# Kernel optimization log

Hardware: AMD Instinct MI355X
Metric: run time of the kernel (lower is better)

## Reference

```python
import jax, jax.numpy as jnp
import numpy as np

NB_KERNEL = 100
DIM_PER_KERNEL = 5


def setup_inputs() -> dict:
    key = jax.random.key(0)
    k1, k2 = jax.random.split(key)
    B, F = 1024, 1024
    x = jax.random.normal(k1, (B, F), dtype=jnp.float32)
    T = jax.random.normal(k2, (F, NB_KERNEL * DIM_PER_KERNEL), dtype=jnp.float32)
    return {"x": x, "T": T}


def reference(x, T):
    B = x.shape[0]
    # project: [B, F] @ [F, K*D] -> [B, K, D]
    m = (x @ T).reshape(B, NB_KERNEL, DIM_PER_KERNEL)
    # pairwise L1 distance over D between all batch rows: [B, K, B]
    # diffs[i, k, d, j] = m[i, k, d] - m[j, k, d]
    diffs = m[:, :, :, None] - jnp.transpose(m, (1, 2, 0))[None, :, :, :]
    l1 = jnp.sum(jnp.abs(diffs), axis=2)  # [B, K, B]
    # exp-kernel similarity summed across batch (includes self term exp(0)=1)
    feat = jnp.sum(jnp.exp(-l1), axis=2)  # [B, K]
    return jnp.concatenate([x, feat], axis=1)  # [B, F + K]
```

## Files before the change

kernel.cpp:

```cpp
#include <hip/hip_runtime.h>
#include <hip/hip_bf16.h>
#include <math.h>

#define B_SZ   1024
#define F_SZ   1024
#define NKER   100
#define DKER   5
#define CCOLS  (NKER * DKER)
#define OUTW   (F_SZ + NKER)
#define LOG2E_F 1.44269504088896340736f

typedef __attribute__((ext_vector_type(8))) short bf16x8;
typedef __attribute__((ext_vector_type(4))) float f32x4;

__device__ __forceinline__ float exp2_hw(float x) {
    float r;
    asm("v_exp_f32 %0, %1" : "=v"(r) : "v"(x));
    return r;
}
__device__ __forceinline__ unsigned cvt_pk_bf16(float lo, float hi) {
    unsigned r;
    asm("v_cvt_pk_bf16_f32 %0, %1, %2" : "=v"(r) : "v"(lo), "v"(hi));
    return r;
}

__global__ __launch_bounds__(256) void init_kernel(const float* __restrict__ x,
                                                   float* __restrict__ out) {
    const int row = blockIdx.x;
    const int t = threadIdx.x;
    const float4 v = *reinterpret_cast<const float4*>(&x[row * F_SZ + t * 4]);
    *reinterpret_cast<float4*>(&out[row * OUTW + t * 4]) = v;
}

__global__ __launch_bounds__(256) void stage_xb_kernel(const float* __restrict__ x,
                                                       short* __restrict__ xb) {
    const int tid = blockIdx.x * 256 + threadIdx.x;
    const int l = tid & 63;
    const int g = tid >> 6;
    const int jt = g >> 5, s = g & 31;
    const int j = jt * 16 + (l & 15);
    const int kb = s * 32 + (l >> 4) * 8;
    const float4 v0 = *reinterpret_cast<const float4*>(&x[j * F_SZ + kb]);
    const float4 v1 = *reinterpret_cast<const float4*>(&x[j * F_SZ + kb + 4]);
    uint4 w;
    w.x = cvt_pk_bf16(v0.x, v0.y);
    w.y = cvt_pk_bf16(v0.z, v0.w);
    w.z = cvt_pk_bf16(v1.x, v1.y);
    w.w = cvt_pk_bf16(v1.z, v1.w);
    *reinterpret_cast<uint4*>(&xb[(size_t)g * 512 + l * 8]) = w;
}

__global__ __launch_bounds__(256) void gemm_frag_kernel(const float* __restrict__ T,
                                                        const short* __restrict__ xb,
                                                        float* __restrict__ mt) {
    const int tid = threadIdx.x;
    const int l = tid & 63;
    const int w = tid >> 6;
    const int tile = blockIdx.x * 4 + w;
    const int ct = tile & 31, jt = tile >> 5;
    const int lr = l & 15;
    const int lk = (l >> 4) * 8;
    const int cA = ct * 16 + lr;
    const int cL = (cA < CCOLS) ? cA : (CCOLS - 1);

    const float* ap = T + (size_t)lk * CCOLS + cL;
    const short* bp = xb + ((size_t)(jt * 32) * 512 + l * 8);

    f32x4 acc = {0.f, 0.f, 0.f, 0.f};
    #pragma unroll 4
    for (int s = 0; s < 32; ++s) {
        const float a0 = ap[0 * CCOLS], a1 = ap[1 * CCOLS];
        const float a2 = ap[2 * CCOLS], a3 = ap[3 * CCOLS];
        const float a4 = ap[4 * CCOLS], a5 = ap[5 * CCOLS];
        const float a6 = ap[6 * CCOLS], a7 = ap[7 * CCOLS];
        const bf16x8 bf = *reinterpret_cast<const bf16x8*>(bp);
        ap += 32 * CCOLS;
        bp += 512;
        union { unsigned u[4]; bf16x8 v; } A;
        A.u[0] = cvt_pk_bf16(a0, a1);
        A.u[1] = cvt_pk_bf16(a2, a3);
        A.u[2] = cvt_pk_bf16(a4, a5);
        A.u[3] = cvt_pk_bf16(a6, a7);
        acc = __builtin_amdgcn_mfma_f32_16x16x32_bf16(A.v, bf, acc, 0, 0, 0);
    }

    const int jst = jt * 16 + lr;
    const int cst = ct * 16 + (l >> 4) * 4;
    #pragma unroll
    for (int q = 0; q < 4; ++q) {
        const int c = cst + q;
        if (c < CCOLS) mt[c * B_SZ + jst] = acc[q] * LOG2E_F;
    }
}

#define GAPAD 40

__global__ __launch_bounds__(512) void gemm_block_kernel(const float* __restrict__ x,
                                                         const float* __restrict__ T,
                                                         float* __restrict__ mt) {
    __shared__ short Al[2][32][GAPAD];
    __shared__ short Bl[2][32][GAPAD];
    __shared__ float red[4][64][4];
    const int tid = threadIdx.x;
    const int l = tid & 63;
    const int w = tid >> 6;
    const int h = tid >> 8;
    const int ht = tid & 255;
    const int c0 = blockIdx.x * 32;
    const int j0 = blockIdx.y * 32;
    const int fh = h * (F_SZ / 2);

    const int sac = ht & 31;
    const int sak = (ht >> 5) * 4;
    const int cldA = (c0 + sac < CCOLS) ? (c0 + sac) : (CCOLS - 1);
    const int sbj = ht >> 3;
    const int sbk = (ht & 7) * 4;

    const int q = w & 3;
    const int cq = (q & 1) * 16;
    const int jq = (q >> 1) * 16;
    const int fr = (l >> 4) * 8;
    const int ar = cq + (l & 15);
    const int br = jq + (l & 15);

    f32x4 acc = {0.f, 0.f, 0.f, 0.f};

    for (int s = 0; s < 16; ++s) {
        const int fb = fh + s * 32;
        const float a0 = T[(fb + sak + 0) * CCOLS + cldA];
        const float a1 = T[(fb + sak + 1) * CCOLS + cldA];
        const float a2 = T[(fb + sak + 2) * CCOLS + cldA];
        const float a3 = T[(fb + sak + 3) * CCOLS + cldA];
        const float4 b = *reinterpret_cast<const float4*>(&x[(j0 + sbj) * F_SZ + fb + sbk]);
        if (s) __syncthreads();
        {
            uint2 aw; aw.x = cvt_pk_bf16(a0, a1); aw.y = cvt_pk_bf16(a2, a3);
            *reinterpret_cast<uint2*>(&Al[h][sac][sak]) = aw;
            uint2 bw; bw.x = cvt_pk_bf16(b.x, b.y); bw.y = cvt_pk_bf16(b.z, b.w);
            *reinterpret_cast<uint2*>(&Bl[h][sbj][sbk]) = bw;
        }
        __syncthreads();
        const bf16x8 af = *reinterpret_cast<const bf16x8*>(&Al[h][ar][fr]);
        const bf16x8 bf = *reinterpret_cast<const bf16x8*>(&Bl[h][br][fr]);
        acc = __builtin_amdgcn_mfma_f32_16x16x32_bf16(af, bf, acc, 0, 0, 0);
    }

    if (h == 1) {
        #pragma unroll
        for (int qq = 0; qq < 4; ++qq) red[q][l][qq] = acc[qq];
    }
    __syncthreads();
    if (h == 0) {
        const int jst = j0 + jq + (l & 15);
        const int cst = c0 + cq + (l >> 4) * 4;
        #pragma unroll
        for (int qq = 0; qq < 4; ++qq) {
            const int c = cst + qq;
            if (c < CCOLS)
                mt[c * B_SZ + jst] = (acc[qq] + red[q][l][qq]) * LOG2E_F;
        }
    }
}

__global__ __launch_bounds__(256) void pair_kernel(const float* __restrict__ mt,
                                                   float* __restrict__ out) {
    __shared__ float red[256];
    const int tid = threadIdx.x;
    const int bx = blockIdx.x;
    const int k = blockIdx.y;
    const int cb = k * DKER;
    const int lane = tid & 63;
    const int wu = __builtin_amdgcn_readfirstlane(tid >> 6);
    const int i = bx * 64 + lane;

    const float a0 = mt[(cb + 0) * B_SZ + i];
    const float a1 = mt[(cb + 1) * B_SZ + i];
    const float a2 = mt[(cb + 2) * B_SZ + i];
    const float a3 = mt[(cb + 3) * B_SZ + i];
    const float a4 = mt[(cb + 4) * B_SZ + i];

    unsigned long long base =
        (unsigned long long)(uintptr_t)(mt + (size_t)cb * B_SZ + wu * 256);

    float acc = 0.f;
    for (int jb = 0; jb < 64; ++jb) {
        f32x4 q0, q1, q2, q3, q4;
        asm("s_load_dwordx4 %0, %[p], 0x0\n\t"
            "s_load_dwordx4 %1, %[p], 0x1000\n\t"
            "s_load_dwordx4 %2, %[p], 0x2000\n\t"
            "s_load_dwordx4 %3, %[p], 0x3000\n\t"
            "s_load_dwordx4 %4, %[p], 0x4000\n\t"
            "s_waitcnt lgkmcnt(0)"
            : "=s"(q0), "=s"(q1), "=s"(q2), "=s"(q3), "=s"(q4)
            : [p] "s"(base));
#define DOJ(E) { \
        const float d0 = q0[E] - a0; \
        const float d1 = q1[E] - a1; \
        const float d2 = q2[E] - a2; \
        const float d3 = q3[E] - a3; \
        const float d4 = q4[E] - a4; \
        const float p01 = fabsf(d0) + fabsf(d1); \
        const float p23 = fabsf(d2) + fabsf(d3); \
        const float p234 = p23 + fabsf(d4); \
        acc += exp2_hw(-p01 - p234); }
        DOJ(0) DOJ(1) DOJ(2) DOJ(3)
#undef DOJ
        base += 16;
    }

    red[tid] = acc;
    __syncthreads();
    if (tid < 64) {
        const float s = red[tid] + red[tid + 64] + red[tid + 128] + red[tid + 192];
        out[(bx * 64 + tid) * OUTW + F_SZ + k] = s;
    }
}

extern "C" void kernel_launch(void* const* d_in, const int* in_sizes, int n_in,
                              void* d_out, int out_size, void* d_ws, size_t ws_size,
                              hipStream_t stream) {
    const float* x = (const float*)d_in[0];
    const float* T = (const float*)d_in[1];
    float* out = (float*)d_out;
    float* mt = (float*)d_ws;
    short* xb = (short*)((char*)d_ws + (size_t)CCOLS * B_SZ * sizeof(float));

    const size_t need = (size_t)CCOLS * B_SZ * sizeof(float)
                      + (size_t)2048 * 512 * sizeof(short);

    init_kernel<<<dim3(B_SZ), 256, 0, stream>>>(x, out);
    if (ws_size >= need) {
        stage_xb_kernel<<<dim3(512), 256, 0, stream>>>(x, xb);
        gemm_frag_kernel<<<dim3(512), 256, 0, stream>>>(T, xb, mt);
    } else {
        gemm_block_kernel<<<dim3(16, 32), 512, 0, stream>>>(x, T, mt);
    }
    pair_kernel<<<dim3(B_SZ / 64, NKER), 256, 0, stream>>>(mt, out);
}
```

Baseline: 115.9 us.

## Pre-stage T into bf16 MFMA fragment layout and widen pair-kernel unrolling

Adds a kernel that transposes T through shared memory and converts it to bf16 MFMA fragments ahead of time, so the GEMM loads packed fragments instead of eight strided fp32 values per step. The pair kernel now loads two groups of scalar vectors per iteration and keeps two accumulators, halving the loop trip count and shortening the dependency chain. The negation is folded into the v_exp operand modifier. The cost is an extra launch and more workspace; if the workspace is too small, the fallback path is taken.

```diff
diff --git a/kernel.cpp b/kernel.cpp
--- a/kernel.cpp
+++ b/kernel.cpp
@@ -13,9 +13,9 @@
 typedef __attribute__((ext_vector_type(8))) short bf16x8;
 typedef __attribute__((ext_vector_type(4))) float f32x4;
 
-__device__ __forceinline__ float exp2_hw(float x) {
+__device__ __forceinline__ float exp2_neg_hw(float x) {
     float r;
-    asm("v_exp_f32 %0, %1" : "=v"(r) : "v"(x));
+    asm("v_exp_f32 %0, -%1" : "=v"(r) : "v"(x));
     return r;
 }
 __device__ __forceinline__ unsigned cvt_pk_bf16(float lo, float hi) {
@@ -50,41 +50,62 @@
     *reinterpret_cast<uint4*>(&xb[(size_t)g * 512 + l * 8]) = w;
 }
 
-__global__ __launch_bounds__(256) void gemm_frag_kernel(const float* __restrict__ T,
-                                                        const short* __restrict__ xb,
-                                                        float* __restrict__ mt) {
+__global__ __launch_bounds__(256) void stage_tb_kernel(const float* __restrict__ T,
+                                                       short* __restrict__ Tb) {
+    __shared__ float Tl[32][72];
+    const int t = threadIdx.x;
+    const int cg = blockIdx.x;
+    const int s = blockIdx.y;
+    const int k0 = s * 32;
+
+    const int kk = t >> 3;
+    const int cc8 = (t & 7) * 8;
+    #pragma unroll
+    for (int e = 0; e < 8; ++e) {
+        int c = cg * 64 + cc8 + e;
+        c = (c < CCOLS) ? c : (CCOLS - 1);
+        Tl[kk][cc8 + e] = T[(k0 + kk) * CCOLS + c];
+    }
+    __syncthreads();
+
+    const int l = t & 63;
+    const int ctl = t >> 6;
+    const int ctg = cg * 4 + ctl;
+    float v[8];
+    #pragma unroll
+    for (int e = 0; e < 8; ++e)
+        v[e] = Tl[(l >> 4) * 8 + e][ctl * 16 + (l & 15)];
+    uint4 w;
+    w.x = cvt_pk_bf16(v[0], v[1]);
+    w.y = cvt_pk_bf16(v[2], v[3]);
+    w.z = cvt_pk_bf16(v[4], v[5]);
+    w.w = cvt_pk_bf16(v[6], v[7]);
+    *reinterpret_cast<uint4*>(&Tb[((size_t)ctg * 32 + s) * 512 + l * 8]) = w;
+}
+
+__global__ __launch_bounds__(256) void gemm_frag2_kernel(const short* __restrict__ Tb,
+                                                         const short* __restrict__ xb,
+                                                         float* __restrict__ mt) {
     const int tid = threadIdx.x;
     const int l = tid & 63;
     const int w = tid >> 6;
     const int tile = blockIdx.x * 4 + w;
     const int ct = tile & 31, jt = tile >> 5;
-    const int lr = l & 15;
-    const int lk = (l >> 4) * 8;
-    const int cA = ct * 16 + lr;
-    const int cL = (cA < CCOLS) ? cA : (CCOLS - 1);
-
-    const float* ap = T + (size_t)lk * CCOLS + cL;
-    const short* bp = xb + ((size_t)(jt * 32) * 512 + l * 8);
+
+    const short* ap = Tb + ((size_t)ct * 32) * 512 + l * 8;
+    const short* bp = xb + ((size_t)jt * 32) * 512 + l * 8;
 
     f32x4 acc = {0.f, 0.f, 0.f, 0.f};
-    #pragma unroll 4
+    #pragma unroll 8
     for (int s = 0; s < 32; ++s) {
-        const float a0 = ap[0 * CCOLS], a1 = ap[1 * CCOLS];
-        const float a2 = ap[2 * CCOLS], a3 = ap[3 * CCOLS];
-        const float a4 = ap[4 * CCOLS], a5 = ap[5 * CCOLS];
-        const float a6 = ap[6 * CCOLS], a7 = ap[7 * CCOLS];
+        const bf16x8 af = *reinterpret_cast<const bf16x8*>(ap);
         const bf16x8 bf = *reinterpret_cast<const bf16x8*>(bp);
-        ap += 32 * CCOLS;
+        ap += 512;
         bp += 512;
-        union { unsigned u[4]; bf16x8 v; } A;
-        A.u[0] = cvt_pk_bf16(a0, a1);
-        A.u[1] = cvt_pk_bf16(a2, a3);
-        A.u[2] = cvt_pk_bf16(a4, a5);
-        A.u[3] = cvt_pk_bf16(a6, a7);
-        acc = __builtin_amdgcn_mfma_f32_16x16x32_bf16(A.v, bf, acc, 0, 0, 0);
-    }
-
-    const int jst = jt * 16 + lr;
+        acc = __builtin_amdgcn_mfma_f32_16x16x32_bf16(af, bf, acc, 0, 0, 0);
+    }
+
+    const int jst = jt * 16 + (l & 15);
     const int cst = ct * 16 + (l >> 4) * 4;
     #pragma unroll
     for (int q = 0; q < 4; ++q) {
@@ -182,33 +203,46 @@
     unsigned long long base =
         (unsigned long long)(uintptr_t)(mt + (size_t)cb * B_SZ + wu * 256);
 
-    float acc = 0.f;
-    for (int jb = 0; jb < 64; ++jb) {
-        f32x4 q0, q1, q2, q3, q4;
+    float accA = 0.f, accB = 0.f;
+    for (int jb = 0; jb < 32; ++jb) {
+        f32x4 q0, q1, q2, q3, q4, q5, q6, q7, q8, q9;
         asm("s_load_dwordx4 %0, %[p], 0x0\n\t"
             "s_load_dwordx4 %1, %[p], 0x1000\n\t"
             "s_load_dwordx4 %2, %[p], 0x2000\n\t"
             "s_load_dwordx4 %3, %[p], 0x3000\n\t"
             "s_load_dwordx4 %4, %[p], 0x4000\n\t"
+            "s_load_dwordx4 %5, %[p], 0x10\n\t"
+            "s_load_dwordx4 %6, %[p], 0x1010\n\t"
+            "s_load_dwordx4 %7, %[p], 0x2010\n\t"
+            "s_load_dwordx4 %8, %[p], 0x3010\n\t"
+            "s_load_dwordx4 %9, %[p], 0x4010\n\t"
             "s_waitcnt lgkmcnt(0)"
-            : "=s"(q0), "=s"(q1), "=s"(q2), "=s"(q3), "=s"(q4)
+            : "=&s"(q0), "=&s"(q1), "=&s"(q2), "=&s"(q3), "=&s"(q4),
+              "=&s"(q5), "=&s"(q6), "=&s"(q7), "=&s"(q8), "=&s"(q9)
             : [p] "s"(base));
-#define DOJ(E) { \
-        const float d0 = q0[E] - a0; \
-        const float d1 = q1[E] - a1; \
-        const float d2 = q2[E] - a2; \
-        const float d3 = q3[E] - a3; \
-        const float d4 = q4[E] - a4; \
+#define DOJ(Q0, Q1, Q2, Q3, Q4, E, ACC) { \
+        const float d0 = Q0[E] - a0; \
+        const float d1 = Q1[E] - a1; \
+        const float d2 = Q2[E] - a2; \
+        const float d3 = Q3[E] - a3; \
+        const float d4 = Q4[E] - a4; \
         const float p01 = fabsf(d0) + fabsf(d1); \
         const float p23 = fabsf(d2) + fabsf(d3); \
         const float p234 = p23 + fabsf(d4); \
-        acc += exp2_hw(-p01 - p234); }
-        DOJ(0) DOJ(1) DOJ(2) DOJ(3)
+        ACC += exp2_neg_hw(p01 + p234); }
+        DOJ(q0, q1, q2, q3, q4, 0, accA)
+        DOJ(q0, q1, q2, q3, q4, 1, accB)
+        DOJ(q0, q1, q2, q3, q4, 2, accA)
+        DOJ(q0, q1, q2, q3, q4, 3, accB)
+        DOJ(q5, q6, q7, q8, q9, 0, accA)
+        DOJ(q5, q6, q7, q8, q9, 1, accB)
+        DOJ(q5, q6, q7, q8, q9, 2, accA)
+        DOJ(q5, q6, q7, q8, q9, 3, accB)
 #undef DOJ
-        base += 16;
-    }
-
-    red[tid] = acc;
+        base += 32;
+    }
+
+    red[tid] = accA + accB;
     __syncthreads();
     if (tid < 64) {
         const float s = red[tid] + red[tid + 64] + red[tid + 128] + red[tid + 192];
@@ -222,16 +256,19 @@
     const float* x = (const float*)d_in[0];
     const float* T = (const float*)d_in[1];
     float* out = (float*)d_out;
+
+    const size_t mt_b = (size_t)CCOLS * B_SZ * sizeof(float);
+    const size_t xb_b = (size_t)2048 * 512 * sizeof(short);
+    const size_t tb_b = (size_t)1024 * 512 * sizeof(short);
     float* mt = (float*)d_ws;
-    short* xb = (short*)((char*)d_ws + (size_t)CCOLS * B_SZ * sizeof(float));
-
-    const size_t need = (size_t)CCOLS * B_SZ * sizeof(float)
-                      + (size_t)2048 * 512 * sizeof(short);
+    short* xb = (short*)((char*)d_ws + mt_b);
+    short* Tb = (short*)((char*)d_ws + mt_b + xb_b);
 
     init_kernel<<<dim3(B_SZ), 256, 0, stream>>>(x, out);
-    if (ws_size >= need) {
+    if (ws_size >= mt_b + xb_b + tb_b) {
         stage_xb_kernel<<<dim3(512), 256, 0, stream>>>(x, xb);
-        gemm_frag_kernel<<<dim3(512), 256, 0, stream>>>(T, xb, mt);
+        stage_tb_kernel<<<dim3(8, 32), 256, 0, stream>>>(T, Tb);
+        gemm_frag2_kernel<<<dim3(512), 256, 0, stream>>>(Tb, xb, mt);
     } else {
         gemm_block_kernel<<<dim3(16, 32), 512, 0, stream>>>(x, T, mt);
     }
```

Result: slower. 118.6 us (+2.3%).
